# Kernel optimization log

Hardware: AMD Instinct MI355X
Metric: run time of the kernel (lower is better)

## Reference

```python
import jax, jax.numpy as jnp
import numpy as np

B, H, S, D = 2, 8, 2048, 64
TEMPERATURE = 8.0  # sqrt(D)

def setup_inputs() -> dict:
    key = jax.random.key(0)
    k1, k2, k3, k4, k5 = jax.random.split(key, 5)
    q = jax.random.normal(k1, (B, H, S, D), dtype=jnp.float32)
    k = jax.random.normal(k2, (B, H, S, D), dtype=jnp.float32)
    v = jax.random.normal(k3, (B, H, S, D), dtype=jnp.float32)
    static_cov = jax.random.normal(k4, (B, S, S), dtype=jnp.float32)
    mask = jax.random.randint(k5, (B, 1, S, S), 0, 2, dtype=jnp.int32)
    # learned parameter: lambda_w initialized to 10 per head, shape [1,H,1,1]
    lambda_w = jnp.full((1, H, 1, 1), 10.0, dtype=jnp.float32)
    return {"q": q, "k": k, "v": v, "static_cov": static_cov,
            "lambda_w": lambda_w, "mask": mask}

def reference(q, k, v, static_cov, lambda_w, mask):
    # blend of scaled QK^T and static covariance bias, convex weights per head
    w_qk = 1.0 / (lambda_w + 1.0)          # [1,H,1,1]
    w_cov = lambda_w / (lambda_w + 1.0)    # [1,H,1,1]
    scores = jnp.einsum('bhsd,bhtd->bhst', q / TEMPERATURE, k)  # [B,H,S,S]
    attn_logits = w_qk * scores + w_cov * static_cov[:, None, :, :]
    attn_logits = jnp.where(mask == 0, jnp.float32(-1e9), attn_logits)
    attn = jax.nn.softmax(attn_logits, axis=-1)  # dropout p=0 -> identity
    output = jnp.einsum('bhst,bhtd->bhsd', attn, v)
    return (output, attn)
```

## Files before the change

### kernel.cpp

```cpp
#include <hip/hip_runtime.h>

#define Bdim 2
#define Hdim 8
#define Sdim 2048
#define Ddim 64
#define PSTR 2056
#define NW 8

typedef short bf16x8 __attribute__((ext_vector_type(8)));
typedef short bf16x4 __attribute__((ext_vector_type(4)));
typedef float f32x4 __attribute__((ext_vector_type(4)));

static __device__ __forceinline__ short f2bf(float x) {
  return __builtin_bit_cast(short, (__bf16)x);
}
static __device__ __forceinline__ float bf2f(short x) {
  unsigned u = ((unsigned)(unsigned short)x) << 16;
  return __builtin_bit_cast(float, u);
}
static __device__ __forceinline__ bf16x8 pack8(float4 a, float4 b, float s) {
  bf16x8 r;
  r[0] = f2bf(a.x * s); r[1] = f2bf(a.y * s);
  r[2] = f2bf(a.z * s); r[3] = f2bf(a.w * s);
  r[4] = f2bf(b.x * s); r[5] = f2bf(b.y * s);
  r[6] = f2bf(b.z * s); r[7] = f2bf(b.w * s);
  return r;
}

__global__ __launch_bounds__(256) void cvt_k(const float* __restrict__ kp,
                                             short* __restrict__ kb) {
  size_t i = ((size_t)blockIdx.x * 256 + threadIdx.x) * 8;
  float4 x0 = *(const float4*)(kp + i);
  float4 x1 = *(const float4*)(kp + i + 4);
  bf16x8 r = pack8(x0, x1, 1.0f);
  *(bf16x8*)(kb + i) = r;
}

__global__ __launch_bounds__(256) void tr_v(const float* __restrict__ vp,
                                            short* __restrict__ vt) {
  __shared__ float tile[64][65];
  const int bh = blockIdx.x >> 5;
  const int t0 = (blockIdx.x & 31) << 6;
  const float* src = vp + ((size_t)bh * Sdim + t0) * Ddim;
  {
    const int tl = threadIdx.x >> 2;
    const int dg = threadIdx.x & 3;
#pragma unroll
    for (int q = 0; q < 4; ++q) {
      float4 x = *(const float4*)(src + tl * Ddim + dg * 16 + q * 4);
      tile[tl][dg * 16 + q * 4 + 0] = x.x;
      tile[tl][dg * 16 + q * 4 + 1] = x.y;
      tile[tl][dg * 16 + q * 4 + 2] = x.z;
      tile[tl][dg * 16 + q * 4 + 3] = x.w;
    }
  }
  __syncthreads();
  {
    const int d  = threadIdx.x >> 2;
    const int tg = threadIdx.x & 3;
    short* dst = vt + ((size_t)bh * Ddim + d) * Sdim + t0 + tg * 16;
    bf16x8 o0, o1;
#pragma unroll
    for (int j = 0; j < 8; ++j) o0[j] = f2bf(tile[tg * 16 + j][d]);
#pragma unroll
    for (int j = 0; j < 8; ++j) o1[j] = f2bf(tile[tg * 16 + 8 + j][d]);
    *(bf16x8*)(dst) = o0;
    *(bf16x8*)(dst + 8) = o1;
  }
}

__global__ __launch_bounds__(256) void cvt_cov(const float* __restrict__ covp,
                                               const int* __restrict__ maskp,
                                               float* __restrict__ cm) {
  const int pair  = blockIdx.x >> 3;
  const int chunk = blockIdx.x & 7;
  const int col   = chunk * 256 + threadIdx.x;
  const size_t rowbase = (size_t)pair * 16;
  float tmp[16];
#pragma unroll
  for (int r = 0; r < 16; ++r) {
    float c = covp[(rowbase + r) * Sdim + col];
    int   m = maskp[(rowbase + r) * Sdim + col];
    tmp[r] = m ? c : -1e9f;
  }
  float* dst = cm + ((size_t)pair * Sdim + col) * 16;
#pragma unroll
  for (int r = 0; r < 16; ++r) dst[r] = tmp[r];
}

#define DECLS(S)                                                               \
  bf16x8 kb0a##S, kb0b##S, kb1a##S, kb1b##S;                                   \
  f32x4 cva##S, cvb##S;

#define LOADS_KCM(S, T0) {                                                     \
    const int _t = (T0);                                                       \
    kb0a##S = *(const bf16x8*)(kbh + (((size_t)(_t + l15)) << 6) + (quad << 3));        \
    kb0b##S = *(const bf16x8*)(kbh + (((size_t)(_t + l15)) << 6) + (quad << 3) + 32);   \
    kb1a##S = *(const bf16x8*)(kbh + (((size_t)(_t + 16 + l15)) << 6) + (quad << 3));      \
    kb1b##S = *(const bf16x8*)(kbh + (((size_t)(_t + 16 + l15)) << 6) + (quad << 3) + 32); \
    cva##S = *(const f32x4*)(cmb + (((size_t)(_t + l15)) << 4) + (quad << 2));        \
    cvb##S = *(const f32x4*)(cmb + (((size_t)(_t + 16 + l15)) << 4) + (quad << 2));   \
  }

#define LOADS_VB(T0) {                                                         \
    const int _t = (T0);                                                       \
    vb0 = *(const bf16x8*)(vtb + (((size_t)(l15))      << 11) + _t + (quad << 3)); \
    vb1 = *(const bf16x8*)(vtb + (((size_t)(16 + l15)) << 11) + _t + (quad << 3)); \
    vb2 = *(const bf16x8*)(vtb + (((size_t)(32 + l15)) << 11) + _t + (quad << 3)); \
    vb3 = *(const bf16x8*)(vtb + (((size_t)(48 + l15)) << 11) + _t + (quad << 3)); \
  }

#define COMPUTE(S, T0) {                                                       \
    f32x4 a0 = {0.f, 0.f, 0.f, 0.f}, a1 = {0.f, 0.f, 0.f, 0.f};               \
    a0 = __builtin_amdgcn_mfma_f32_16x16x32_bf16(aq0, kb0a##S, a0, 0, 0, 0);   \
    a0 = __builtin_amdgcn_mfma_f32_16x16x32_bf16(aq1, kb0b##S, a0, 0, 0, 0);   \
    a1 = __builtin_amdgcn_mfma_f32_16x16x32_bf16(aq0, kb1a##S, a1, 0, 0, 0);   \
    a1 = __builtin_amdgcn_mfma_f32_16x16x32_bf16(aq1, kb1b##S, a1, 0, 0, 0);   \
    const int col0 = (T0) + l15;                                               \
    const int row0 = quad * 4;                                                 \
    _Pragma("unroll") for (int r = 0; r < 4; ++r) {                            \
      float p0 = __expf(a0[r] + w_cov * cva##S[r]);                            \
      float p1 = __expf(a1[r] + w_cov * cvb##S[r]);                            \
      lsum[r] += p0 + p1;                                                      \
      Pl[row0 + r][col0]      = f2bf(p0);                                      \
      Pl[row0 + r][col0 + 16] = f2bf(p1);                                      \
    }                                                                          \
    bf16x8 pa = *(const bf16x8*)&Pl[l15][(T0) + quad * 8];                     \
    oacc0 = __builtin_amdgcn_mfma_f32_16x16x32_bf16(pa, vb0, oacc0, 0, 0, 0);  \
    oacc1 = __builtin_amdgcn_mfma_f32_16x16x32_bf16(pa, vb1, oacc1, 0, 0, 0);  \
    oacc2 = __builtin_amdgcn_mfma_f32_16x16x32_bf16(pa, vb2, oacc2, 0, 0, 0);  \
    oacc3 = __builtin_amdgcn_mfma_f32_16x16x32_bf16(pa, vb3, oacc3, 0, 0, 0);  \
  }

__global__ __launch_bounds__(512, 4) void fused_attn(
    const float* __restrict__ qp, const short* __restrict__ kbp,
    const short* __restrict__ vtp, const float* __restrict__ cmp,
    const float* __restrict__ lamp,
    float* __restrict__ outO, float* __restrict__ outA)
{
  __shared__ __align__(16) short Pl[16][PSTR];
  __shared__ float Ls[NW][16];
  __shared__ float Lrow[16];

  const int tid  = threadIdx.x;
  const int wv   = tid >> 6;
  const int lane = tid & 63;
  const int quad = lane >> 4;
  const int l15  = lane & 15;

  const int bid = blockIdx.x;
  const int h  = bid & 7;
  const int qt = (bid >> 3) & 127;
  const int b  = bid >> 10;

  const float lam   = lamp[h];
  const float w_qk  = 1.0f / (lam + 1.0f);
  const float w_cov = lam / (lam + 1.0f);
  const float qscale = w_qk * 0.125f;

  const int q0 = qt * 16;
  const int bh = b * Hdim + h;

  const float* qbase = qp + ((size_t)bh * Sdim + q0) * Ddim;
  const short* kbh   = kbp + (size_t)bh * Sdim * Ddim;
  const short* vtb   = vtp + (size_t)bh * Ddim * Sdim;
  const float* cmb   = cmp + ((size_t)(b * 128 + qt)) * Sdim * 16;
  float* oA = outA + ((size_t)bh * Sdim + q0) * (size_t)Sdim;
  float* oO = outO + ((size_t)bh * Sdim + q0) * Ddim;

  bf16x8 aq0, aq1;
  {
    const float* qr = qbase + l15 * Ddim + quad * 8;
    float4 x0 = *(const float4*)(qr);
    float4 x1 = *(const float4*)(qr + 4);
    aq0 = pack8(x0, x1, qscale);
    float4 y0 = *(const float4*)(qr + 32);
    float4 y1 = *(const float4*)(qr + 36);
    aq1 = pack8(y0, y1, qscale);
  }

  const int tbeg = wv * (Sdim / NW);
  const int tend = tbeg + (Sdim / NW);

  float lsum[4] = {0.f, 0.f, 0.f, 0.f};
  f32x4 oacc0 = {0.f, 0.f, 0.f, 0.f}, oacc1 = {0.f, 0.f, 0.f, 0.f};
  f32x4 oacc2 = {0.f, 0.f, 0.f, 0.f}, oacc3 = {0.f, 0.f, 0.f, 0.f};
  bf16x8 vb0, vb1, vb2, vb3;

  DECLS(E)
  DECLS(O)
  LOADS_KCM(E, tbeg)
#pragma unroll 1
  for (int t0 = tbeg; t0 < tend; t0 += 64) {
    LOADS_VB(t0)
    LOADS_KCM(O, t0 + 32)
    COMPUTE(E, t0)
    const int tnx = (t0 + 64 < tend) ? (t0 + 64) : tbeg;
    LOADS_VB(t0 + 32)
    LOADS_KCM(E, tnx)
    COMPUTE(O, t0 + 32)
  }

#pragma unroll
  for (int r = 0; r < 4; ++r) {
    float s = lsum[r];
    s += __shfl_xor(s, 1, 16);
    s += __shfl_xor(s, 2, 16);
    s += __shfl_xor(s, 4, 16);
    s += __shfl_xor(s, 8, 16);
    if (l15 == 0) Ls[wv][quad * 4 + r] = s;
  }
  __syncthreads();
  if (tid < 16) {
    float s = 0.f;
#pragma unroll
    for (int w2 = 0; w2 < NW; ++w2) s += Ls[w2][tid];
    Lrow[tid] = 1.0f / s;
  }
  __syncthreads();

#pragma unroll 1
  for (int row = 0; row < 16; ++row) {
    const float rinv = Lrow[row];
    float* orow = oA + (size_t)row * Sdim;
    const int c0 = tbeg + lane * 4;
    bf16x4 pv = *(const bf16x4*)&Pl[row][c0];
    f32x4 o;
    o[0] = bf2f(pv[0]) * rinv;
    o[1] = bf2f(pv[1]) * rinv;
    o[2] = bf2f(pv[2]) * rinv;
    o[3] = bf2f(pv[3]) * rinv;
    __builtin_nontemporal_store(o, (f32x4*)&orow[c0]);
  }
  __syncthreads();

  float* Ored = (float*)&Pl[0][0];
#pragma unroll
  for (int r = 0; r < 4; ++r) {
    Ored[((wv * 64 + lane) * 16) + 0  + r] = oacc0[r];
    Ored[((wv * 64 + lane) * 16) + 4  + r] = oacc1[r];
    Ored[((wv * 64 + lane) * 16) + 8  + r] = oacc2[r];
    Ored[((wv * 64 + lane) * 16) + 12 + r] = oacc3[r];
  }
  __syncthreads();
  if (wv < 4) {
#pragma unroll
    for (int r = 0; r < 4; ++r) {
      float s = 0.f;
#pragma unroll
      for (int w2 = 0; w2 < NW; ++w2)
        s += Ored[((w2 * 64 + lane) * 16) + wv * 4 + r];
      const int row = quad * 4 + r;
      __builtin_nontemporal_store(s * Lrow[row], &oO[row * Ddim + wv * 16 + l15]);
    }
  }
}

extern "C" void kernel_launch(void* const* d_in, const int* in_sizes, int n_in,
                              void* d_out, int out_size, void* d_ws, size_t ws_size,
                              hipStream_t stream) {
  const float* q    = (const float*)d_in[0];
  const float* k    = (const float*)d_in[1];
  const float* v    = (const float*)d_in[2];
  const float* cov  = (const float*)d_in[3];
  const float* lam  = (const float*)d_in[4];
  const int*   mask = (const int*)d_in[5];
  float* outO = (float*)d_out;
  float* outA = outO + (size_t)Bdim * Hdim * Sdim * Ddim;

  short* kb = (short*)d_ws;
  short* vt = kb + (size_t)Bdim * Hdim * Sdim * Ddim;
  float* cm = (float*)(vt + (size_t)Bdim * Hdim * Sdim * Ddim);
  (void)ws_size;

  cvt_k<<<dim3((Bdim * Hdim * Sdim * Ddim) / (256 * 8)), 256, 0, stream>>>(k, kb);
  tr_v<<<dim3(Bdim * Hdim * (Sdim / 64)), 256, 0, stream>>>(v, vt);
  cvt_cov<<<dim3(Bdim * (Sdim / 16) * 8), 256, 0, stream>>>(cov, mask, cm);

  dim3 grid(Bdim * Hdim * (Sdim / 16));
  fused_attn<<<grid, 512, 0, stream>>>(q, kb, vt, cm, lam, outO, outA);
}
```

Measured before the change: 468.5 us.

## Store masked covariance as bf16 and fully unroll attention loop with deeper prefetch

The premasked covariance workspace is now written and read as bf16 instead of fp32, halving its traffic in both the conversion kernel and the fused attention kernel. The per-wave key loop over 256 columns is fully unrolled, with double-buffered K and V registers and triple-buffered covariance loads issued further ahead of use. The aim is to cut memory bandwidth and hide load latency better. The cost is higher register pressure under the 512x4 launch bounds and a small precision loss in the covariance bias.

```diff
diff --git a/kernel.cpp b/kernel.cpp
--- a/kernel.cpp
+++ b/kernel.cpp
@@ -71,70 +71,80 @@
 
 __global__ __launch_bounds__(256) void cvt_cov(const float* __restrict__ covp,
                                                const int* __restrict__ maskp,
-                                               float* __restrict__ cm) {
+                                               short* __restrict__ cm) {
   const int pair  = blockIdx.x >> 3;
   const int chunk = blockIdx.x & 7;
   const int col   = chunk * 256 + threadIdx.x;
   const size_t rowbase = (size_t)pair * 16;
-  float tmp[16];
-#pragma unroll
-  for (int r = 0; r < 16; ++r) {
+  bf16x8 o0, o1;
+#pragma unroll
+  for (int r = 0; r < 8; ++r) {
     float c = covp[(rowbase + r) * Sdim + col];
     int   m = maskp[(rowbase + r) * Sdim + col];
-    tmp[r] = m ? c : -1e9f;
-  }
-  float* dst = cm + ((size_t)pair * Sdim + col) * 16;
-#pragma unroll
-  for (int r = 0; r < 16; ++r) dst[r] = tmp[r];
-}
-
-#define DECLS(S)                                                               \
-  bf16x8 kb0a##S, kb0b##S, kb1a##S, kb1b##S;                                   \
-  f32x4 cva##S, cvb##S;
-
-#define LOADS_KCM(S, T0) {                                                     \
+    o0[r] = f2bf(m ? c : -1e9f);
+  }
+#pragma unroll
+  for (int r = 0; r < 8; ++r) {
+    float c = covp[(rowbase + 8 + r) * Sdim + col];
+    int   m = maskp[(rowbase + 8 + r) * Sdim + col];
+    o1[r] = f2bf(m ? c : -1e9f);
+  }
+  short* dst = cm + ((size_t)pair * Sdim + col) * 16;
+  *(bf16x8*)(dst) = o0;
+  *(bf16x8*)(dst + 8) = o1;
+}
+
+#define DECL_K(S) bf16x8 k0a##S, k0b##S, k1a##S, k1b##S;
+#define DECL_V(S) bf16x8 v0##S, v1##S, v2##S, v3##S;
+#define DECL_C(S) bf16x4 ca##S, cb##S;
+
+#define LK(S, T0) {                                                            \
     const int _t = (T0);                                                       \
-    kb0a##S = *(const bf16x8*)(kbh + (((size_t)(_t + l15)) << 6) + (quad << 3));        \
-    kb0b##S = *(const bf16x8*)(kbh + (((size_t)(_t + l15)) << 6) + (quad << 3) + 32);   \
-    kb1a##S = *(const bf16x8*)(kbh + (((size_t)(_t + 16 + l15)) << 6) + (quad << 3));      \
-    kb1b##S = *(const bf16x8*)(kbh + (((size_t)(_t + 16 + l15)) << 6) + (quad << 3) + 32); \
-    cva##S = *(const f32x4*)(cmb + (((size_t)(_t + l15)) << 4) + (quad << 2));        \
-    cvb##S = *(const f32x4*)(cmb + (((size_t)(_t + 16 + l15)) << 4) + (quad << 2));   \
-  }
-
-#define LOADS_VB(T0) {                                                         \
+    k0a##S = *(const bf16x8*)(kbh + (((size_t)(_t + l15)) << 6) + (quad << 3));        \
+    k0b##S = *(const bf16x8*)(kbh + (((size_t)(_t + l15)) << 6) + (quad << 3) + 32);   \
+    k1a##S = *(const bf16x8*)(kbh + (((size_t)(_t + 16 + l15)) << 6) + (quad << 3));      \
+    k1b##S = *(const bf16x8*)(kbh + (((size_t)(_t + 16 + l15)) << 6) + (quad << 3) + 32); \
+  }
+
+#define LV(S, T0) {                                                            \
     const int _t = (T0);                                                       \
-    vb0 = *(const bf16x8*)(vtb + (((size_t)(l15))      << 11) + _t + (quad << 3)); \
-    vb1 = *(const bf16x8*)(vtb + (((size_t)(16 + l15)) << 11) + _t + (quad << 3)); \
-    vb2 = *(const bf16x8*)(vtb + (((size_t)(32 + l15)) << 11) + _t + (quad << 3)); \
-    vb3 = *(const bf16x8*)(vtb + (((size_t)(48 + l15)) << 11) + _t + (quad << 3)); \
-  }
-
-#define COMPUTE(S, T0) {                                                       \
+    v0##S = *(const bf16x8*)(vtb + (((size_t)(l15))      << 11) + _t + (quad << 3)); \
+    v1##S = *(const bf16x8*)(vtb + (((size_t)(16 + l15)) << 11) + _t + (quad << 3)); \
+    v2##S = *(const bf16x8*)(vtb + (((size_t)(32 + l15)) << 11) + _t + (quad << 3)); \
+    v3##S = *(const bf16x8*)(vtb + (((size_t)(48 + l15)) << 11) + _t + (quad << 3)); \
+  }
+
+#define LC(S, T0) {                                                            \
+    const int _t = (T0);                                                       \
+    ca##S = *(const bf16x4*)(cmb + (((size_t)(_t + l15)) << 4) + (quad << 2));      \
+    cb##S = *(const bf16x4*)(cmb + (((size_t)(_t + 16 + l15)) << 4) + (quad << 2)); \
+  }
+
+#define BODY(KS, VS, CS, T0) {                                                 \
     f32x4 a0 = {0.f, 0.f, 0.f, 0.f}, a1 = {0.f, 0.f, 0.f, 0.f};               \
-    a0 = __builtin_amdgcn_mfma_f32_16x16x32_bf16(aq0, kb0a##S, a0, 0, 0, 0);   \
-    a0 = __builtin_amdgcn_mfma_f32_16x16x32_bf16(aq1, kb0b##S, a0, 0, 0, 0);   \
-    a1 = __builtin_amdgcn_mfma_f32_16x16x32_bf16(aq0, kb1a##S, a1, 0, 0, 0);   \
-    a1 = __builtin_amdgcn_mfma_f32_16x16x32_bf16(aq1, kb1b##S, a1, 0, 0, 0);   \
+    a0 = __builtin_amdgcn_mfma_f32_16x16x32_bf16(aq0, k0a##KS, a0, 0, 0, 0);   \
+    a0 = __builtin_amdgcn_mfma_f32_16x16x32_bf16(aq1, k0b##KS, a0, 0, 0, 0);   \
+    a1 = __builtin_amdgcn_mfma_f32_16x16x32_bf16(aq0, k1a##KS, a1, 0, 0, 0);   \
+    a1 = __builtin_amdgcn_mfma_f32_16x16x32_bf16(aq1, k1b##KS, a1, 0, 0, 0);   \
     const int col0 = (T0) + l15;                                               \
     const int row0 = quad * 4;                                                 \
     _Pragma("unroll") for (int r = 0; r < 4; ++r) {                            \
-      float p0 = __expf(a0[r] + w_cov * cva##S[r]);                            \
-      float p1 = __expf(a1[r] + w_cov * cvb##S[r]);                            \
+      float p0 = __expf(a0[r] + w_cov * bf2f(ca##CS[r]));                      \
+      float p1 = __expf(a1[r] + w_cov * bf2f(cb##CS[r]));                      \
       lsum[r] += p0 + p1;                                                      \
       Pl[row0 + r][col0]      = f2bf(p0);                                      \
       Pl[row0 + r][col0 + 16] = f2bf(p1);                                      \
     }                                                                          \
     bf16x8 pa = *(const bf16x8*)&Pl[l15][(T0) + quad * 8];                     \
-    oacc0 = __builtin_amdgcn_mfma_f32_16x16x32_bf16(pa, vb0, oacc0, 0, 0, 0);  \
-    oacc1 = __builtin_amdgcn_mfma_f32_16x16x32_bf16(pa, vb1, oacc1, 0, 0, 0);  \
-    oacc2 = __builtin_amdgcn_mfma_f32_16x16x32_bf16(pa, vb2, oacc2, 0, 0, 0);  \
-    oacc3 = __builtin_amdgcn_mfma_f32_16x16x32_bf16(pa, vb3, oacc3, 0, 0, 0);  \
+    oacc0 = __builtin_amdgcn_mfma_f32_16x16x32_bf16(pa, v0##VS, oacc0, 0, 0, 0); \
+    oacc1 = __builtin_amdgcn_mfma_f32_16x16x32_bf16(pa, v1##VS, oacc1, 0, 0, 0); \
+    oacc2 = __builtin_amdgcn_mfma_f32_16x16x32_bf16(pa, v2##VS, oacc2, 0, 0, 0); \
+    oacc3 = __builtin_amdgcn_mfma_f32_16x16x32_bf16(pa, v3##VS, oacc3, 0, 0, 0); \
   }
 
 __global__ __launch_bounds__(512, 4) void fused_attn(
     const float* __restrict__ qp, const short* __restrict__ kbp,
-    const short* __restrict__ vtp, const float* __restrict__ cmp,
+    const short* __restrict__ vtp, const short* __restrict__ cmp,
     const float* __restrict__ lamp,
     float* __restrict__ outO, float* __restrict__ outA)
 {
@@ -164,7 +174,7 @@
   const float* qbase = qp + ((size_t)bh * Sdim + q0) * Ddim;
   const short* kbh   = kbp + (size_t)bh * Sdim * Ddim;
   const short* vtb   = vtp + (size_t)bh * Ddim * Sdim;
-  const float* cmb   = cmp + ((size_t)(b * 128 + qt)) * Sdim * 16;
+  const short* cmb   = cmp + ((size_t)(b * 128 + qt)) * Sdim * 16;
   float* oA = outA + ((size_t)bh * Sdim + q0) * (size_t)Sdim;
   float* oO = outO + ((size_t)bh * Sdim + q0) * Ddim;
 
@@ -179,27 +189,25 @@
     aq1 = pack8(y0, y1, qscale);
   }
 
-  const int tbeg = wv * (Sdim / NW);
-  const int tend = tbeg + (Sdim / NW);
+  const int t = wv * (Sdim / NW);
 
   float lsum[4] = {0.f, 0.f, 0.f, 0.f};
   f32x4 oacc0 = {0.f, 0.f, 0.f, 0.f}, oacc1 = {0.f, 0.f, 0.f, 0.f};
   f32x4 oacc2 = {0.f, 0.f, 0.f, 0.f}, oacc3 = {0.f, 0.f, 0.f, 0.f};
-  bf16x8 vb0, vb1, vb2, vb3;
-
-  DECLS(E)
-  DECLS(O)
-  LOADS_KCM(E, tbeg)
-#pragma unroll 1
-  for (int t0 = tbeg; t0 < tend; t0 += 64) {
-    LOADS_VB(t0)
-    LOADS_KCM(O, t0 + 32)
-    COMPUTE(E, t0)
-    const int tnx = (t0 + 64 < tend) ? (t0 + 64) : tbeg;
-    LOADS_VB(t0 + 32)
-    LOADS_KCM(E, tnx)
-    COMPUTE(O, t0 + 32)
-  }
+
+  DECL_K(A) DECL_K(B)
+  DECL_V(X) DECL_V(Y)
+  DECL_C(c0) DECL_C(c1) DECL_C(c2)
+
+  LK(A, t)         LV(X, t)         LC(c0, t)        LC(c1, t + 32)
+  LK(B, t + 32)    LV(Y, t + 32)    LC(c2, t + 64)   BODY(A, X, c0, t)
+  LK(A, t + 64)    LV(X, t + 64)    LC(c0, t + 96)   BODY(B, Y, c1, t + 32)
+  LK(B, t + 96)    LV(Y, t + 96)    LC(c1, t + 128)  BODY(A, X, c2, t + 64)
+  LK(A, t + 128)   LV(X, t + 128)   LC(c2, t + 160)  BODY(B, Y, c0, t + 96)
+  LK(B, t + 160)   LV(Y, t + 160)   LC(c0, t + 192)  BODY(A, X, c1, t + 128)
+  LK(A, t + 192)   LV(X, t + 192)   LC(c1, t + 224)  BODY(B, Y, c2, t + 160)
+  LK(B, t + 224)   LV(Y, t + 224)                    BODY(A, X, c0, t + 192)
+                                                     BODY(B, Y, c1, t + 224)
 
 #pragma unroll
   for (int r = 0; r < 4; ++r) {
@@ -223,7 +231,7 @@
   for (int row = 0; row < 16; ++row) {
     const float rinv = Lrow[row];
     float* orow = oA + (size_t)row * Sdim;
-    const int c0 = tbeg + lane * 4;
+    const int c0 = t + lane * 4;
     bf16x4 pv = *(const bf16x4*)&Pl[row][c0];
     f32x4 o;
     o[0] = bf2f(pv[0]) * rinv;
@@ -270,7 +278,7 @@
 
   short* kb = (short*)d_ws;
   short* vt = kb + (size_t)Bdim * Hdim * Sdim * Ddim;
-  float* cm = (float*)(vt + (size_t)Bdim * Hdim * Sdim * Ddim);
+  short* cm = vt + (size_t)Bdim * Hdim * Sdim * Ddim;
   (void)ws_size;
 
   cvt_k<<<dim3((Bdim * Hdim * Sdim * Ddim) / (256 * 8)), 256, 0, stream>>>(k, kb);
```

New measurement: 458.2 us. 2.2% less time.
